# Optimization experiments

Measured on AMD Instinct MI355X. Metric: run time of the kernel, lower is better.

Reference implementation:

```python
import jax, jax.numpy as jnp
import numpy as np

N_HEAD = 16
HEAD_DIM = 64  # n_embd // n_head = 1024 // 16


def setup_inputs() -> dict:
    key = jax.random.key(0)
    k1, k2, k3 = jax.random.split(key, 3)
    B, S, D = 2, 2048, 1024
    x = jax.random.normal(k1, (B, S, D), dtype=jnp.float32)
    # torch nn.Linear stores weight [out, in]; we keep [in, out] for x @ W
    w_qkv = jax.random.normal(k2, (D, 3 * D), dtype=jnp.float32) * (D ** -0.5)
    w_proj = jax.random.normal(k3, (D, D), dtype=jnp.float32) * (D ** -0.5)
    return {"x": x, "w_qkv": w_qkv, "w_proj": w_proj}


def reference(x, w_qkv, w_proj):
    B, S, D = x.shape
    qkv = x @ w_qkv  # [B, S, 3D]
    q, k, v = jnp.split(qkv, 3, axis=-1)
    # [B, H, S, hd]
    q = q.reshape(B, S, N_HEAD, HEAD_DIM).transpose(0, 2, 1, 3)
    k = k.reshape(B, S, N_HEAD, HEAD_DIM).transpose(0, 2, 1, 3)
    v = v.reshape(B, S, N_HEAD, HEAD_DIM).transpose(0, 2, 1, 3)
    att = jnp.einsum('bhid,bhjd->bhij', q, k) * (HEAD_DIM ** -0.5)
    causal = jnp.tril(jnp.ones((S, S), dtype=bool))
    att = jnp.where(causal, att, jnp.finfo(att.dtype).min)
    att = jax.nn.softmax(att, axis=-1)
    # dropout p=0 (eval) -> identity
    y = jnp.einsum('bhij,bhjd->bhid', att, v)
    y = y.transpose(0, 2, 1, 3).reshape(B, S, D)
    return y @ w_proj
```

## Files before the change

### kernel.cpp

```cpp
#include <hip/hip_runtime.h>

#define AS1 __attribute__((address_space(1)))
#define AS3 __attribute__((address_space(3)))

using f32x4 = __attribute__((ext_vector_type(4))) float;
using s16x8 = __attribute__((ext_vector_type(8))) short;
using u16x4 = __attribute__((ext_vector_type(4))) unsigned short;

__device__ __forceinline__ unsigned short f2bf(float f) {
  union { float f; unsigned u; } v; v.f = f;
  unsigned u = v.u;
  return (unsigned short)((u + 0x7FFFu + ((u >> 16) & 1u)) >> 16);
}

__device__ __forceinline__ unsigned short f2bf_trunc(float f) {
  union { float f; unsigned u; } v; v.f = f;
  return (unsigned short)(v.u >> 16);
}

__device__ __forceinline__ void load_lds16(const void* g, void* l) {
  __builtin_amdgcn_global_load_lds((const AS1 void*)g, (AS3 void*)l, 16, 0, 0);
}

__global__ __launch_bounds__(256) void prep_kernel(const float* __restrict__ x,
                                                   const float* __restrict__ w_qkv,
                                                   const float* __restrict__ w_proj,
                                                   unsigned short* __restrict__ xb,
                                                   unsigned short* __restrict__ wqkvT,
                                                   unsigned short* __restrict__ wprojT) {
  __shared__ float tile[32][33];
  const int bid = blockIdx.x, tid = threadIdx.x;
  if (bid < 4096) {
    int i = bid * 256 + tid;
    float4 v = ((const float4*)x)[i];
    u16x4 o;
    o.x = f2bf(v.x); o.y = f2bf(v.y); o.z = f2bf(v.z); o.w = f2bf(v.w);
    ((u16x4*)xb)[i] = o;
    return;
  }
  const float* in;
  unsigned short* out;
  int bx, by, R, C;
  if (bid < 7168) {
    int t = bid - 4096;
    bx = t % 96; by = t / 96; R = 1024; C = 3072;
    in = w_qkv; out = wqkvT;
  } else {
    int t = bid - 7168;
    bx = t % 32; by = t / 32; R = 1024; C = 1024;
    in = w_proj; out = wprojT;
  }
  const int tx = tid & 31, ty = tid >> 5;
  int xcol = bx * 32 + tx;
  int y0 = by * 32;
  for (int j = ty; j < 32; j += 8)
    tile[j][tx] = in[(size_t)(y0 + j) * C + xcol];
  __syncthreads();
  int x2 = by * 32 + tx;
  int y2 = bx * 32;
  for (int j = ty; j < 32; j += 8)
    out[(size_t)(y2 + j) * R + x2] = f2bf(tile[tx][j]);
}

__global__ __launch_bounds__(256) void transpose_v(const unsigned short* __restrict__ qkv,
                                                   unsigned short* __restrict__ Vt) {
  __shared__ unsigned short tile[64][65];
  const int tid = threadIdx.x;
  const int bh = blockIdx.y, b = bh >> 4, h = bh & 15;
  const int s0 = blockIdx.x * 64;
#pragma unroll
  for (int it = 0; it < 2; ++it) {
    int c = tid + it * 256;
    int row = c >> 3, cc = c & 7;
    s16x8 v = *(const s16x8*)(qkv + (size_t)(b * 2048 + s0 + row) * 3072 + 2048 + h * 64 + cc * 8);
#pragma unroll
    for (int j = 0; j < 8; ++j) tile[row][cc * 8 + j] = (unsigned short)v[j];
  }
  __syncthreads();
#pragma unroll
  for (int it = 0; it < 2; ++it) {
    int c = tid + it * 256;
    int d = c >> 3, sc = c & 7;
    s16x8 o;
#pragma unroll
    for (int j = 0; j < 8; ++j) o[j] = (short)tile[sc * 8 + j][d];
    *(s16x8*)(Vt + (size_t)bh * 64 * 2048 + (size_t)d * 2048 + s0 + sc * 8) = o;
  }
}

__global__ __launch_bounds__(256) void gemm_qkv(const unsigned short* __restrict__ A,
                                                const unsigned short* __restrict__ Bt,
                                                unsigned short* __restrict__ C,
                                                int M, int N, int K) {
  __shared__ unsigned short As[128 * 32];
  __shared__ unsigned short Bs[128 * 32];
  const int tid = threadIdx.x;
  const int wave = tid >> 6, lane = tid & 63;
  const int l15 = lane & 15, quad = lane >> 4;
  const int wm = wave & 1, wn = wave >> 1;
  const int bm = blockIdx.y, bn = blockIdx.x;

  f32x4 acc[4][4] = {};

  const int c0 = wave * 128 + lane;
  for (int k0 = 0; k0 < K; k0 += 32) {
    __syncthreads();
#pragma unroll
    for (int s = 0; s < 2; ++s) {
      int c = c0 + s * 64;
      int row = c >> 2, kc = (c & 3) * 8;
      load_lds16(A + (size_t)(bm * 128 + row) * K + k0 + kc, As + c * 8);
      load_lds16(Bt + (size_t)(bn * 128 + row) * K + k0 + kc, Bs + c * 8);
    }
    __syncthreads();
    s16x8 af[4], bfr[4];
#pragma unroll
    for (int i = 0; i < 4; ++i) {
      af[i]  = *(const s16x8*)(As + (wm * 64 + i * 16 + l15) * 32 + quad * 8);
      bfr[i] = *(const s16x8*)(Bs + (wn * 64 + i * 16 + l15) * 32 + quad * 8);
    }
#pragma unroll
    for (int i = 0; i < 4; ++i)
#pragma unroll
      for (int j = 0; j < 4; ++j)
        acc[i][j] = __builtin_amdgcn_mfma_f32_16x16x32_bf16(af[i], bfr[j], acc[i][j], 0, 0, 0);
  }

  const int row0 = bm * 128 + wm * 64 + quad * 4;
  const int col0 = bn * 128 + wn * 64 + l15;
#pragma unroll
  for (int i = 0; i < 4; ++i)
#pragma unroll
    for (int j = 0; j < 4; ++j)
#pragma unroll
      for (int r = 0; r < 4; ++r)
        C[(size_t)(row0 + i * 16 + r) * N + (col0 + j * 16)] = f2bf(acc[i][j][r]);
}

__global__ __launch_bounds__(256) void gemm_proj(const unsigned short* __restrict__ A,
                                                 const unsigned short* __restrict__ Bt,
                                                 float* __restrict__ C,
                                                 int M, int N, int K) {
  __shared__ unsigned short As[128 * 32];
  __shared__ unsigned short Bs[64 * 32];
  const int tid = threadIdx.x;
  const int wave = tid >> 6, lane = tid & 63;
  const int l15 = lane & 15, quad = lane >> 4;
  const int wm = wave & 1, wn = wave >> 1;
  const int bm = blockIdx.y, bn = blockIdx.x;

  f32x4 acc[4][2] = {};

  for (int k0 = 0; k0 < K; k0 += 32) {
    __syncthreads();
#pragma unroll
    for (int s = 0; s < 2; ++s) {
      int c = tid + s * 256;
      int row = c >> 2, kc = (c & 3) * 8;
      load_lds16(A + (size_t)(bm * 128 + row) * K + k0 + kc, As + c * 8);
    }
    {
      int c = tid;
      int row = c >> 2, kc = (c & 3) * 8;
      load_lds16(Bt + (size_t)(bn * 64 + row) * K + k0 + kc, Bs + c * 8);
    }
    __syncthreads();
    s16x8 af[4], bfr[2];
#pragma unroll
    for (int i = 0; i < 4; ++i)
      af[i] = *(const s16x8*)(As + (wm * 64 + i * 16 + l15) * 32 + quad * 8);
#pragma unroll
    for (int j = 0; j < 2; ++j)
      bfr[j] = *(const s16x8*)(Bs + (wn * 32 + j * 16 + l15) * 32 + quad * 8);
#pragma unroll
    for (int i = 0; i < 4; ++i)
#pragma unroll
      for (int j = 0; j < 2; ++j)
        acc[i][j] = __builtin_amdgcn_mfma_f32_16x16x32_bf16(af[i], bfr[j], acc[i][j], 0, 0, 0);
  }

  const int row0 = bm * 128 + wm * 64 + quad * 4;
  const int col0 = bn * 64 + wn * 32 + l15;
#pragma unroll
  for (int i = 0; i < 4; ++i)
#pragma unroll
    for (int j = 0; j < 2; ++j)
#pragma unroll
      for (int r = 0; r < 4; ++r)
        C[(size_t)(row0 + i * 16 + r) * N + (col0 + j * 16)] = acc[i][j][r];
}

__global__ __launch_bounds__(512) void attn_kernel(const unsigned short* __restrict__ qkv,
                                                   const unsigned short* __restrict__ Vt,
                                                   unsigned short* __restrict__ Y) {
  __shared__ unsigned short Qs[128 * 64];
  __shared__ unsigned short Ks[64 * 64];
  __shared__ unsigned short Vs[64 * 64];
  const int tid = threadIdx.x;
  const int wave = tid >> 6, lane = tid & 63;
  const int l15 = lane & 15, quad = lane >> 4;
  const int sx = l15 & 7;

  const int p = blockIdx.x;
  const int r_ = p >> 8, c_ = p & 255;
  const int m_ = c_ & 15, g_ = c_ >> 4;
  const int bh = g_ + 16 * r_;
  const int lq = r_ ? (15 - m_) : m_;
  const int q0 = lq * 128;
  const int b = bh >> 4, h = bh & 15;
  const size_t base = (size_t)b * 2048 * 3072 + h * 64;
  const size_t vbase = (size_t)bh * 64 * 2048;

#pragma unroll
  for (int s = 0; s < 2; ++s) {
    int cid = tid + s * 512;
    int row = cid >> 3, cc = cid & 7;
    int kc = (cc ^ (row & 7)) * 8;
    load_lds16(qkv + base + (size_t)(q0 + row) * 3072 + kc, Qs + cid * 8);
  }
  __syncthreads();
  const int qr = wave * 16 + l15;
  s16x8 qf[2];
  qf[0] = *(const s16x8*)(Qs + qr * 64 + ((quad    ) ^ sx) * 8);
  qf[1] = *(const s16x8*)(Qs + qr * 64 + ((quad + 4) ^ sx) * 8);

  f32x4 o[4] = {};
  float m_i[4] = {-1e30f, -1e30f, -1e30f, -1e30f};
  float l_i[4] = {0.f, 0.f, 0.f, 0.f};
  const float kScale = 0.125f * 1.44269504f;
  const int qrow_w0 = q0 + wave * 16;
  unsigned short* Pw = Qs + wave * 16 * 64;

  for (int j0 = 0; j0 <= q0 + 64; j0 += 64) {
    __syncthreads();
    {
      int row = tid >> 3, cc = tid & 7;
      int kc = (cc ^ (row & 7)) * 8;
      load_lds16(qkv + base + (size_t)(j0 + row) * 3072 + 1024 + kc, Ks + tid * 8);
      load_lds16(Vt + vbase + (size_t)row * 2048 + j0 + kc, Vs + tid * 8);
    }
    __syncthreads();

    if (j0 <= qrow_w0 + 15) {
      f32x4 s[4];
#pragma unroll
      for (int nt = 0; nt < 4; ++nt) {
        const int kr = nt * 16 + l15;
        s16x8 kf0 = *(const s16x8*)(Ks + kr * 64 + ((quad    ) ^ sx) * 8);
        s16x8 kf1 = *(const s16x8*)(Ks + kr * 64 + ((quad + 4) ^ sx) * 8);
        f32x4 z = {};
        z = __builtin_amdgcn_mfma_f32_16x16x32_bf16(qf[0], kf0, z, 0, 0, 0);
        z = __builtin_amdgcn_mfma_f32_16x16x32_bf16(qf[1], kf1, z, 0, 0, 0);
        s[nt] = z;
      }

      if (j0 + 63 > qrow_w0) {
        const int qrow = qrow_w0 + quad * 4;
#pragma unroll
        for (int nt = 0; nt < 4; ++nt) {
          int key = j0 + nt * 16 + l15;
#pragma unroll
          for (int r = 0; r < 4; ++r)
            if (key > qrow + r) s[nt][r] = -3e38f;
        }
      }

      float tmax[4], alpha[4], rsum[4], mk[4];
#pragma unroll
      for (int r = 0; r < 4; ++r)
        tmax[r] = fmaxf(fmaxf(s[0][r], s[1][r]), fmaxf(s[2][r], s[3][r]));
#pragma unroll
      for (int off = 1; off < 16; off <<= 1)
#pragma unroll
        for (int r = 0; r < 4; ++r)
          tmax[r] = fmaxf(tmax[r], __shfl_xor(tmax[r], off, 64));
#pragma unroll
      for (int r = 0; r < 4; ++r) {
        float mn = fmaxf(m_i[r], tmax[r]);
        alpha[r] = __builtin_amdgcn_exp2f((m_i[r] - mn) * kScale);
        m_i[r] = mn;
        mk[r] = mn * kScale;
        rsum[r] = 0.f;
      }
#pragma unroll
      for (int nt = 0; nt < 4; ++nt)
#pragma unroll
        for (int r = 0; r < 4; ++r) {
          float pv = __builtin_amdgcn_exp2f(__builtin_fmaf(s[nt][r], kScale, -mk[r]));
          s[nt][r] = pv;
          rsum[r] += pv;
        }
#pragma unroll
      for (int off = 1; off < 16; off <<= 1)
#pragma unroll
        for (int r = 0; r < 4; ++r)
          rsum[r] += __shfl_xor(rsum[r], off, 64);
#pragma unroll
      for (int r = 0; r < 4; ++r)
        l_i[r] = l_i[r] * alpha[r] + rsum[r];
#pragma unroll
      for (int dt = 0; dt < 4; ++dt)
#pragma unroll
        for (int r = 0; r < 4; ++r)
          o[dt][r] *= alpha[r];

      const int l15h = l15 >> 3, l15l = l15 & 7;
#pragma unroll
      for (int nt = 0; nt < 4; ++nt)
#pragma unroll
        for (int r = 0; r < 4; ++r) {
          int prow = quad * 4 + r;
          Pw[prow * 64 + ((2 * nt + l15h) ^ (prow & 7)) * 8 + l15l] = f2bf_trunc(s[nt][r]);
        }

      s16x8 pf[2];
      pf[0] = *(const s16x8*)(Pw + l15 * 64 + ((quad    ) ^ sx) * 8);
      pf[1] = *(const s16x8*)(Pw + l15 * 64 + ((quad + 4) ^ sx) * 8);

#pragma unroll
      for (int dt = 0; dt < 4; ++dt) {
        const int vr = dt * 16 + l15;
#pragma unroll
        for (int kk = 0; kk < 2; ++kk) {
          s16x8 vf = *(const s16x8*)(Vs + vr * 64 + ((quad + 4 * kk) ^ sx) * 8);
          o[dt] = __builtin_amdgcn_mfma_f32_16x16x32_bf16(pf[kk], vf, o[dt], 0, 0, 0);
        }
      }
    }
  }

#pragma unroll
  for (int r = 0; r < 4; ++r)
    l_i[r] = 1.0f / l_i[r];
  const size_t yrow = (size_t)(b * 2048 + qrow_w0 + quad * 4);
#pragma unroll
  for (int dt = 0; dt < 4; ++dt)
#pragma unroll
    for (int r = 0; r < 4; ++r)
      Y[(yrow + r) * 1024 + h * 64 + dt * 16 + l15] = f2bf(o[dt][r] * l_i[r]);
}

extern "C" void kernel_launch(void* const* d_in, const int* in_sizes, int n_in,
                              void* d_out, int out_size, void* d_ws, size_t ws_size,
                              hipStream_t stream) {
  const float* x      = (const float*)d_in[0];
  const float* w_qkv  = (const float*)d_in[1];
  const float* w_proj = (const float*)d_in[2];
  char* ws = (char*)d_ws;
  unsigned short* xb     = (unsigned short*)(ws);
  unsigned short* wqkvT  = (unsigned short*)(ws + (size_t)(8  << 20));
  unsigned short* wprojT = (unsigned short*)(ws + (size_t)(14 << 20));
  unsigned short* qkv    = (unsigned short*)(ws + (size_t)(16 << 20));
  unsigned short* y      = (unsigned short*)(ws + (size_t)(40 << 20));
  unsigned short* Vt     = (unsigned short*)(ws + (size_t)(48 << 20));

  prep_kernel<<<8192, 256, 0, stream>>>(x, w_qkv, w_proj, xb, wqkvT, wprojT);
  gemm_qkv<<<dim3(24, 32), 256, 0, stream>>>(xb, wqkvT, qkv, 4096, 3072, 1024);
  transpose_v<<<dim3(32, 32), 256, 0, stream>>>(qkv, Vt);
  attn_kernel<<<512, 512, 0, stream>>>(qkv, Vt, y);
  gemm_proj<<<dim3(16, 32), 256, 0, stream>>>(y, wprojT, (float*)d_out, 4096, 1024, 1024);
}
```

Baseline: 208.6 us.

## Transpose attention MFMA operands, double GEMM K-step with swizzled LDS

The attention kernel swaps the MFMA operand order so each lane owns one query row, not four. That shrinks the row max and sum reductions from four 16-lane shuffle trees to two cross-quad shuffles, and lets P be written to LDS as packed 8-byte stores and Y stored as 4-element vectors. Both GEMMs now stage a K-tile of 64 instead of 32 with an XOR-swizzled LDS layout, which halves the barrier count per K and is meant to avoid bank conflicts. The cost is twice the LDS per block, which may lower occupancy.

```diff
diff --git a/kernel.cpp b/kernel.cpp
--- a/kernel.cpp
+++ b/kernel.cpp
@@ -6,6 +6,7 @@
 using f32x4 = __attribute__((ext_vector_type(4))) float;
 using s16x8 = __attribute__((ext_vector_type(8))) short;
 using u16x4 = __attribute__((ext_vector_type(4))) unsigned short;
+using u32x2 = __attribute__((ext_vector_type(2))) unsigned int;
 
 __device__ __forceinline__ unsigned short f2bf(float f) {
   union { float f; unsigned u; } v; v.f = f;
@@ -13,9 +14,9 @@
   return (unsigned short)((u + 0x7FFFu + ((u >> 16) & 1u)) >> 16);
 }
 
-__device__ __forceinline__ unsigned short f2bf_trunc(float f) {
-  union { float f; unsigned u; } v; v.f = f;
-  return (unsigned short)(v.u >> 16);
+__device__ __forceinline__ unsigned pack_bf2(float a, float b) {
+  union { float f; unsigned u; } x, y; x.f = a; y.f = b;
+  return (x.u >> 16) | (y.u & 0xFFFF0000u);
 }
 
 __device__ __forceinline__ void load_lds16(const void* g, void* l) {
@@ -92,38 +93,42 @@
                                                 const unsigned short* __restrict__ Bt,
                                                 unsigned short* __restrict__ C,
                                                 int M, int N, int K) {
-  __shared__ unsigned short As[128 * 32];
-  __shared__ unsigned short Bs[128 * 32];
+  __shared__ unsigned short As[128 * 64];
+  __shared__ unsigned short Bs[128 * 64];
   const int tid = threadIdx.x;
   const int wave = tid >> 6, lane = tid & 63;
   const int l15 = lane & 15, quad = lane >> 4;
+  const int sx = l15 & 7;
   const int wm = wave & 1, wn = wave >> 1;
   const int bm = blockIdx.y, bn = blockIdx.x;
 
   f32x4 acc[4][4] = {};
 
-  const int c0 = wave * 128 + lane;
-  for (int k0 = 0; k0 < K; k0 += 32) {
-    __syncthreads();
-#pragma unroll
-    for (int s = 0; s < 2; ++s) {
-      int c = c0 + s * 64;
-      int row = c >> 2, kc = (c & 3) * 8;
+  for (int k0 = 0; k0 < K; k0 += 64) {
+    __syncthreads();
+#pragma unroll
+    for (int s = 0; s < 4; ++s) {
+      int c = tid + s * 256;
+      int row = c >> 3, cc = c & 7;
+      int kc = (cc ^ (row & 7)) * 8;
       load_lds16(A + (size_t)(bm * 128 + row) * K + k0 + kc, As + c * 8);
       load_lds16(Bt + (size_t)(bn * 128 + row) * K + k0 + kc, Bs + c * 8);
     }
     __syncthreads();
-    s16x8 af[4], bfr[4];
-#pragma unroll
-    for (int i = 0; i < 4; ++i) {
-      af[i]  = *(const s16x8*)(As + (wm * 64 + i * 16 + l15) * 32 + quad * 8);
-      bfr[i] = *(const s16x8*)(Bs + (wn * 64 + i * 16 + l15) * 32 + quad * 8);
-    }
-#pragma unroll
-    for (int i = 0; i < 4; ++i)
-#pragma unroll
-      for (int j = 0; j < 4; ++j)
-        acc[i][j] = __builtin_amdgcn_mfma_f32_16x16x32_bf16(af[i], bfr[j], acc[i][j], 0, 0, 0);
+#pragma unroll
+    for (int kk = 0; kk < 2; ++kk) {
+      s16x8 af[4], bfr[4];
+#pragma unroll
+      for (int i = 0; i < 4; ++i) {
+        af[i]  = *(const s16x8*)(As + (wm * 64 + i * 16 + l15) * 64 + ((quad + 4 * kk) ^ sx) * 8);
+        bfr[i] = *(const s16x8*)(Bs + (wn * 64 + i * 16 + l15) * 64 + ((quad + 4 * kk) ^ sx) * 8);
+      }
+#pragma unroll
+      for (int i = 0; i < 4; ++i)
+#pragma unroll
+        for (int j = 0; j < 4; ++j)
+          acc[i][j] = __builtin_amdgcn_mfma_f32_16x16x32_bf16(af[i], bfr[j], acc[i][j], 0, 0, 0);
+    }
   }
 
   const int row0 = bm * 128 + wm * 64 + quad * 4;
@@ -141,42 +146,49 @@
                                                  const unsigned short* __restrict__ Bt,
                                                  float* __restrict__ C,
                                                  int M, int N, int K) {
-  __shared__ unsigned short As[128 * 32];
-  __shared__ unsigned short Bs[64 * 32];
+  __shared__ unsigned short As[128 * 64];
+  __shared__ unsigned short Bs[64 * 64];
   const int tid = threadIdx.x;
   const int wave = tid >> 6, lane = tid & 63;
   const int l15 = lane & 15, quad = lane >> 4;
+  const int sx = l15 & 7;
   const int wm = wave & 1, wn = wave >> 1;
   const int bm = blockIdx.y, bn = blockIdx.x;
 
   f32x4 acc[4][2] = {};
 
-  for (int k0 = 0; k0 < K; k0 += 32) {
-    __syncthreads();
+  for (int k0 = 0; k0 < K; k0 += 64) {
+    __syncthreads();
+#pragma unroll
+    for (int s = 0; s < 4; ++s) {
+      int c = tid + s * 256;
+      int row = c >> 3, cc = c & 7;
+      int kc = (cc ^ (row & 7)) * 8;
+      load_lds16(A + (size_t)(bm * 128 + row) * K + k0 + kc, As + c * 8);
+    }
 #pragma unroll
     for (int s = 0; s < 2; ++s) {
       int c = tid + s * 256;
-      int row = c >> 2, kc = (c & 3) * 8;
-      load_lds16(A + (size_t)(bm * 128 + row) * K + k0 + kc, As + c * 8);
-    }
-    {
-      int c = tid;
-      int row = c >> 2, kc = (c & 3) * 8;
+      int row = c >> 3, cc = c & 7;
+      int kc = (cc ^ (row & 7)) * 8;
       load_lds16(Bt + (size_t)(bn * 64 + row) * K + k0 + kc, Bs + c * 8);
     }
     __syncthreads();
-    s16x8 af[4], bfr[2];
-#pragma unroll
-    for (int i = 0; i < 4; ++i)
-      af[i] = *(const s16x8*)(As + (wm * 64 + i * 16 + l15) * 32 + quad * 8);
-#pragma unroll
-    for (int j = 0; j < 2; ++j)
-      bfr[j] = *(const s16x8*)(Bs + (wn * 32 + j * 16 + l15) * 32 + quad * 8);
-#pragma unroll
-    for (int i = 0; i < 4; ++i)
+#pragma unroll
+    for (int kk = 0; kk < 2; ++kk) {
+      s16x8 af[4], bfr[2];
+#pragma unroll
+      for (int i = 0; i < 4; ++i)
+        af[i] = *(const s16x8*)(As + (wm * 64 + i * 16 + l15) * 64 + ((quad + 4 * kk) ^ sx) * 8);
 #pragma unroll
       for (int j = 0; j < 2; ++j)
-        acc[i][j] = __builtin_amdgcn_mfma_f32_16x16x32_bf16(af[i], bfr[j], acc[i][j], 0, 0, 0);
+        bfr[j] = *(const s16x8*)(Bs + (wn * 32 + j * 16 + l15) * 64 + ((quad + 4 * kk) ^ sx) * 8);
+#pragma unroll
+      for (int i = 0; i < 4; ++i)
+#pragma unroll
+        for (int j = 0; j < 2; ++j)
+          acc[i][j] = __builtin_amdgcn_mfma_f32_16x16x32_bf16(af[i], bfr[j], acc[i][j], 0, 0, 0);
+    }
   }
 
   const int row0 = bm * 128 + wm * 64 + quad * 4;
@@ -199,7 +211,7 @@
   const int tid = threadIdx.x;
   const int wave = tid >> 6, lane = tid & 63;
   const int l15 = lane & 15, quad = lane >> 4;
-  const int sx = l15 & 7;
+  const int sx = l15 & 7, sx2 = sx << 1;
 
   const int p = blockIdx.x;
   const int r_ = p >> 8, c_ = p & 255;
@@ -219,16 +231,15 @@
     load_lds16(qkv + base + (size_t)(q0 + row) * 3072 + kc, Qs + cid * 8);
   }
   __syncthreads();
-  const int qr = wave * 16 + l15;
   s16x8 qf[2];
-  qf[0] = *(const s16x8*)(Qs + qr * 64 + ((quad    ) ^ sx) * 8);
-  qf[1] = *(const s16x8*)(Qs + qr * 64 + ((quad + 4) ^ sx) * 8);
+  qf[0] = *(const s16x8*)(Qs + (wave * 16 + l15) * 64 + ((quad    ) ^ sx) * 8);
+  qf[1] = *(const s16x8*)(Qs + (wave * 16 + l15) * 64 + ((quad + 4) ^ sx) * 8);
 
   f32x4 o[4] = {};
-  float m_i[4] = {-1e30f, -1e30f, -1e30f, -1e30f};
-  float l_i[4] = {0.f, 0.f, 0.f, 0.f};
+  float m_i = -1e30f, l_i = 0.f;
   const float kScale = 0.125f * 1.44269504f;
   const int qrow_w0 = q0 + wave * 16;
+  const int qrow = qrow_w0 + l15;
   unsigned short* Pw = Qs + wave * 16 * 64;
 
   for (int j0 = 0; j0 <= q0 + 64; j0 += 64) {
@@ -249,95 +260,84 @@
         s16x8 kf0 = *(const s16x8*)(Ks + kr * 64 + ((quad    ) ^ sx) * 8);
         s16x8 kf1 = *(const s16x8*)(Ks + kr * 64 + ((quad + 4) ^ sx) * 8);
         f32x4 z = {};
-        z = __builtin_amdgcn_mfma_f32_16x16x32_bf16(qf[0], kf0, z, 0, 0, 0);
-        z = __builtin_amdgcn_mfma_f32_16x16x32_bf16(qf[1], kf1, z, 0, 0, 0);
+        z = __builtin_amdgcn_mfma_f32_16x16x32_bf16(kf0, qf[0], z, 0, 0, 0);
+        z = __builtin_amdgcn_mfma_f32_16x16x32_bf16(kf1, qf[1], z, 0, 0, 0);
         s[nt] = z;
       }
 
       if (j0 + 63 > qrow_w0) {
-        const int qrow = qrow_w0 + quad * 4;
 #pragma unroll
         for (int nt = 0; nt < 4; ++nt) {
-          int key = j0 + nt * 16 + l15;
+          int key0 = j0 + nt * 16 + quad * 4;
 #pragma unroll
           for (int r = 0; r < 4; ++r)
-            if (key > qrow + r) s[nt][r] = -3e38f;
+            if (key0 + r > qrow) s[nt][r] = -3e38f;
         }
       }
 
-      float tmax[4], alpha[4], rsum[4], mk[4];
-#pragma unroll
-      for (int r = 0; r < 4; ++r)
-        tmax[r] = fmaxf(fmaxf(s[0][r], s[1][r]), fmaxf(s[2][r], s[3][r]));
-#pragma unroll
-      for (int off = 1; off < 16; off <<= 1)
+      float tmax = s[0][0];
+#pragma unroll
+      for (int nt = 0; nt < 4; ++nt)
 #pragma unroll
         for (int r = 0; r < 4; ++r)
-          tmax[r] = fmaxf(tmax[r], __shfl_xor(tmax[r], off, 64));
-#pragma unroll
-      for (int r = 0; r < 4; ++r) {
-        float mn = fmaxf(m_i[r], tmax[r]);
-        alpha[r] = __builtin_amdgcn_exp2f((m_i[r] - mn) * kScale);
-        m_i[r] = mn;
-        mk[r] = mn * kScale;
-        rsum[r] = 0.f;
-      }
+          tmax = fmaxf(tmax, s[nt][r]);
+      tmax = fmaxf(tmax, __shfl_xor(tmax, 16, 64));
+      tmax = fmaxf(tmax, __shfl_xor(tmax, 32, 64));
+      float mn = fmaxf(m_i, tmax);
+      float alpha = __builtin_amdgcn_exp2f((m_i - mn) * kScale);
+      m_i = mn;
+      const float mk = mn * kScale;
+      float rsum = 0.f;
 #pragma unroll
       for (int nt = 0; nt < 4; ++nt)
 #pragma unroll
         for (int r = 0; r < 4; ++r) {
-          float pv = __builtin_amdgcn_exp2f(__builtin_fmaf(s[nt][r], kScale, -mk[r]));
+          float pv = __builtin_amdgcn_exp2f(__builtin_fmaf(s[nt][r], kScale, -mk));
           s[nt][r] = pv;
-          rsum[r] += pv;
+          rsum += pv;
         }
-#pragma unroll
-      for (int off = 1; off < 16; off <<= 1)
+      rsum += __shfl_xor(rsum, 16, 64);
+      rsum += __shfl_xor(rsum, 32, 64);
+      l_i = l_i * alpha + rsum;
+#pragma unroll
+      for (int dt = 0; dt < 4; ++dt)
 #pragma unroll
         for (int r = 0; r < 4; ++r)
-          rsum[r] += __shfl_xor(rsum[r], off, 64);
-#pragma unroll
-      for (int r = 0; r < 4; ++r)
-        l_i[r] = l_i[r] * alpha[r] + rsum[r];
-#pragma unroll
-      for (int dt = 0; dt < 4; ++dt)
-#pragma unroll
-        for (int r = 0; r < 4; ++r)
-          o[dt][r] *= alpha[r];
-
-      const int l15h = l15 >> 3, l15l = l15 & 7;
-#pragma unroll
-      for (int nt = 0; nt < 4; ++nt)
-#pragma unroll
-        for (int r = 0; r < 4; ++r) {
-          int prow = quad * 4 + r;
-          Pw[prow * 64 + ((2 * nt + l15h) ^ (prow & 7)) * 8 + l15l] = f2bf_trunc(s[nt][r]);
-        }
+          o[dt][r] *= alpha;
+
+#pragma unroll
+      for (int nt = 0; nt < 4; ++nt) {
+        u32x2 pk;
+        pk.x = pack_bf2(s[nt][0], s[nt][1]);
+        pk.y = pack_bf2(s[nt][2], s[nt][3]);
+        int phys = (nt * 4 + quad) ^ sx2;
+        *(u32x2*)(Pw + l15 * 64 + phys * 4) = pk;
+      }
 
       s16x8 pf[2];
-      pf[0] = *(const s16x8*)(Pw + l15 * 64 + ((quad    ) ^ sx) * 8);
-      pf[1] = *(const s16x8*)(Pw + l15 * 64 + ((quad + 4) ^ sx) * 8);
+      pf[0] = *(const s16x8*)(Pw + l15 * 64 + (((quad * 2)    ) ^ sx2) * 4);
+      pf[1] = *(const s16x8*)(Pw + l15 * 64 + (((quad * 2) + 8) ^ sx2) * 4);
 
 #pragma unroll
       for (int dt = 0; dt < 4; ++dt) {
         const int vr = dt * 16 + l15;
-#pragma unroll
-        for (int kk = 0; kk < 2; ++kk) {
-          s16x8 vf = *(const s16x8*)(Vs + vr * 64 + ((quad + 4 * kk) ^ sx) * 8);
-          o[dt] = __builtin_amdgcn_mfma_f32_16x16x32_bf16(pf[kk], vf, o[dt], 0, 0, 0);
-        }
-      }
-    }
-  }
-
-#pragma unroll
-  for (int r = 0; r < 4; ++r)
-    l_i[r] = 1.0f / l_i[r];
-  const size_t yrow = (size_t)(b * 2048 + qrow_w0 + quad * 4);
-#pragma unroll
-  for (int dt = 0; dt < 4; ++dt)
-#pragma unroll
-    for (int r = 0; r < 4; ++r)
-      Y[(yrow + r) * 1024 + h * 64 + dt * 16 + l15] = f2bf(o[dt][r] * l_i[r]);
+        s16x8 vf0 = *(const s16x8*)(Vs + vr * 64 + ((quad    ) ^ sx) * 8);
+        s16x8 vf1 = *(const s16x8*)(Vs + vr * 64 + ((quad + 4) ^ sx) * 8);
+        o[dt] = __builtin_amdgcn_mfma_f32_16x16x32_bf16(vf0, pf[0], o[dt], 0, 0, 0);
+        o[dt] = __builtin_amdgcn_mfma_f32_16x16x32_bf16(vf1, pf[1], o[dt], 0, 0, 0);
+      }
+    }
+  }
+
+  const float inv = 1.0f / l_i;
+  const size_t yoff = (size_t)(b * 2048 + qrow) * 1024 + h * 64 + quad * 4;
+#pragma unroll
+  for (int dt = 0; dt < 4; ++dt) {
+    u16x4 pk;
+#pragma unroll
+    for (int r = 0; r < 4; ++r) pk[r] = f2bf(o[dt][r] * inv);
+    *(u16x4*)(Y + yoff + dt * 16) = pk;
+  }
 }
 
 extern "C" void kernel_launch(void* const* d_in, const int* in_sizes, int n_in,
```

Result: faster. 182.9 us (-12.3%).
